# Performance work log

Hardware: AMD Instinct MI355X
Metric: run time of the kernel (lower is better)

The kernel has to match this reference:

```python
import jax, jax.numpy as jnp
import numpy as np

TAU = 0.07
EPS = 1e-6
LN_EPS = 1e-5  # torch nn.LayerNorm default
NORM_EPS = 1e-12  # torch F.normalize default


def _l2norm(x):
    n = jnp.sqrt(jnp.sum(x * x, axis=-1, keepdims=True))
    return x / jnp.maximum(n, NORM_EPS)


def setup_inputs() -> dict:
    key = jax.random.key(0)
    k1, k2, k3, k4 = jax.random.split(key, 4)
    B, N, D, K = 16, 2048, 512, 8
    f_raw = jax.random.normal(k1, (B, N, D), dtype=jnp.float32)
    f_q = jax.random.normal(k2, (B, D), dtype=jnp.float32)
    gt_mask = jax.random.randint(k3, (B, N), 0, 2) > 0
    q_bg = jax.random.normal(k4, (K, D), dtype=jnp.float32) * 0.02
    alpha = jnp.float32(1.0)
    ln_w = jnp.ones((D,), dtype=jnp.float32)
    ln_b = jnp.zeros((D,), dtype=jnp.float32)
    return {"f_raw": f_raw, "f_q": f_q, "gt_mask": gt_mask,
            "q_bg": q_bg, "alpha": alpha, "ln_w": ln_w, "ln_b": ln_b}


def reference(f_raw, f_q, gt_mask, q_bg, alpha, ln_w, ln_b):
    B, N, D = f_raw.shape
    # background prototypes via cross-attention (K queries)
    attn = jax.nn.softmax(jnp.einsum('kd,bnd->bkn', q_bg, f_raw) / jnp.sqrt(jnp.float32(D)), axis=-1)
    p_bg = jnp.einsum('bkn,bnd->bkd', attn, f_raw)  # [B,K,D]
    # projection of each token onto each prototype, summed (einsum instead of (B,N,K,D) broadcast)
    numer = jnp.einsum('bnd,bkd->bnk', f_raw, p_bg)
    denom = jnp.sum(p_bg * p_bg, axis=-1) + EPS        # [B,K]
    coef = numer / denom[:, None, :]                   # [B,N,K]
    f_bg = jnp.einsum('bnk,bkd->bnd', coef, p_bg)      # [B,N,D]
    # foreground = LayerNorm(f_raw - alpha * f_bg)
    x = f_raw - alpha * f_bg
    mu = jnp.mean(x, axis=-1, keepdims=True)
    var = jnp.mean((x - mu) ** 2, axis=-1, keepdims=True)
    f_fg = (x - mu) / jnp.sqrt(var + LN_EPS) * ln_w + ln_b
    # semantic scores vs query embedding
    sim = jnp.sum(_l2norm(f_fg) * _l2norm(f_q)[:, None, :], axis=-1)
    s_sem = jax.nn.sigmoid(sim / TAU)
    # compactness: min cosine distance of each token to a prototype
    dot = jnp.einsum('bnd,bkd->bnk', _l2norm(f_raw), _l2norm(p_bg))
    loss_compact = jnp.mean(jnp.min(1.0 - dot, axis=-1))
    # orthogonality: off-diagonal gram of normalized f_bg ([B,N,N])
    p_n = _l2norm(f_bg)
    gram = jnp.einsum('bnd,bmd->bnm', p_n, p_n)
    eye = jnp.eye(N, dtype=gram.dtype)[None]
    loss_orth = jnp.mean((gram * (1.0 - eye)) ** 2)
    # alignment: -log of positive scores (masked mean)
    m = gt_mask.astype(s_sem.dtype)
    cnt = jnp.sum(m)
    neg_log = -jnp.log(jnp.maximum(s_sem, EPS))
    loss_align = jnp.where(cnt > 0, jnp.sum(neg_log * m) / jnp.maximum(cnt, 1.0), 0.0)
    return f_fg, f_bg, p_bg, s_sem, loss_compact, loss_orth, loss_align
```

## Files before the change

kernel.cpp:

```cpp
#include <hip/hip_runtime.h>
#include <math.h>

#define Bb 16
#define Nn 2048
#define Dd 512
#define Kk 8

constexpr float TAU = 0.07f;
constexpr float EPSc = 1e-6f;
constexpr float LN_EPS = 1e-5f;
constexpr float NORM_EPS = 1e-12f;
constexpr float SCALE = 0.04419417382415922f;

constexpr size_t OUT_FFG  = 0;
constexpr size_t OUT_FBG  = (size_t)Bb*Nn*Dd;
constexpr size_t OUT_PBG  = OUT_FBG + (size_t)Bb*Nn*Dd;
constexpr size_t OUT_SSEM = OUT_PBG + (size_t)Bb*Kk*Dd;
constexpr size_t OUT_LOSS = OUT_SSEM + (size_t)Bb*Nn;

constexpr int    NCH = 64;
constexpr size_t WS_PBPART = 0;
constexpr size_t WS_SUMW   = WS_PBPART + (size_t)Bb*NCH*Kk*Dd;
constexpr size_t WS_NF2    = WS_SUMW + (size_t)Bb*NCH*Kk;
constexpr size_t WS_SF     = WS_NF2 + (size_t)Bb*Nn;
constexpr size_t WS_M      = WS_SF + (size_t)Bb*Nn;
constexpr size_t WS_IDEN   = WS_M + Bb*64;
constexpr size_t WS_INP    = WS_IDEN + Bb*Kk;
constexpr size_t WS_P1     = WS_INP + Bb*Kk;
constexpr size_t WS_FQN    = WS_P1 + Bb*Kk;
constexpr size_t WS_CP     = WS_FQN + (size_t)Bb*Dd;
constexpr size_t WS_P5A    = WS_CP + (size_t)Bb*Nn*Kk;
constexpr size_t WS_P5B    = WS_P5A + 2048;
constexpr size_t WS_TRB    = WS_P5B + 2048;

__device__ __forceinline__ float dot4(float4 a, float4 b) {
    return a.x*b.x + a.y*b.y + a.z*b.z + a.w*b.w;
}
__device__ __forceinline__ float4 add4(float4 a, float4 b) {
    return make_float4(a.x+b.x, a.y+b.y, a.z+b.z, a.w+b.w);
}
__device__ __forceinline__ float4 shfl_xor4(float4 v, int m) {
    return make_float4(__shfl_xor(v.x,m,64), __shfl_xor(v.y,m,64),
                       __shfl_xor(v.z,m,64), __shfl_xor(v.w,m,64));
}
__device__ __forceinline__ float4 shfl4(float4 v, int src) {
    return make_float4(__shfl(v.x,src,64), __shfl(v.y,src,64),
                       __shfl(v.z,src,64), __shfl(v.w,src,64));
}

__global__ __launch_bounds__(512, 4) void k1_scores(const float* __restrict__ f_raw,
                                                    const float* __restrict__ q_bg,
                                                    float* __restrict__ ws) {
    int b = blockIdx.x >> 6;
    int chunk = blockIdx.x & 63;
    int tok0 = chunk * 32;
    int tid = threadIdx.x, lane = tid & 63, wave = tid >> 6;
    __shared__ float qls[Kk*Dd];
    __shared__ float part[8][32][12];
    __shared__ float wlds[32][8];
    __shared__ float swsum[8][8];
    for (int e = tid; e < Kk*Dd; e += 512) qls[e] = q_bg[e];
    __syncthreads();
    int tok = lane & 31, half = lane >> 5;
    int dwl = wave*64 + half*32;
    const float* ftok = f_raw + ((size_t)b*Nn + tok0 + tok)*Dd + dwl;

    float a[8] = {0,0,0,0,0,0,0,0};
    float nf2 = 0.f, sf = 0.f;
    #pragma unroll
    for (int cc = 0; cc < 8; ++cc) {
        float4 f4 = *(const float4*)(ftok + cc*4);
        int qo = dwl + cc*4;
        #pragma unroll
        for (int k = 0; k < 8; ++k) {
            float4 q4 = *(const float4*)&qls[k*Dd + qo];
            a[k] += dot4(f4, q4);
        }
        nf2 += dot4(f4, f4);
        sf  += f4.x + f4.y + f4.z + f4.w;
    }
    #pragma unroll
    for (int k = 0; k < 8; ++k) a[k] += __shfl_xor(a[k], 32, 64);
    nf2 += __shfl_xor(nf2, 32, 64);
    sf  += __shfl_xor(sf, 32, 64);
    if (lane < 32) {
        *(float4*)&part[wave][tok][0] = make_float4(a[0],a[1],a[2],a[3]);
        *(float4*)&part[wave][tok][4] = make_float4(a[4],a[5],a[6],a[7]);
        *(float2*)&part[wave][tok][8] = make_float2(nf2, sf);
    }
    __syncthreads();
    {
        int sub = lane >> 4, idx = lane & 15;
        int pw = idx >> 1, hh = idx & 1;
        int tokl = wave*4 + sub;
        float4 Av = *(const float4*)&part[pw][tokl][hh*4];
        Av = add4(Av, shfl_xor4(Av, 2));
        Av = add4(Av, shfl_xor4(Av, 4));
        Av = add4(Av, shfl_xor4(Av, 8));
        int gbase = lane & 48;
        float4 Alo = shfl4(Av, gbase);
        float4 Ahi = shfl4(Av, gbase + 1);
        float n2 = (idx < 8) ? part[idx][tokl][8] : 0.f;
        float s1 = (idx < 8) ? part[idx][tokl][9] : 0.f;
        #pragma unroll
        for (int m = 1; m <= 8; m <<= 1) {
            n2 += __shfl_xor(n2, m, 64);
            s1 += __shfl_xor(s1, m, 64);
        }
        float w8[8];
        w8[0]=expf(Alo.x*SCALE); w8[1]=expf(Alo.y*SCALE);
        w8[2]=expf(Alo.z*SCALE); w8[3]=expf(Alo.w*SCALE);
        w8[4]=expf(Ahi.x*SCALE); w8[5]=expf(Ahi.y*SCALE);
        w8[6]=expf(Ahi.z*SCALE); w8[7]=expf(Ahi.w*SCALE);
        if (idx == 0) {
            size_t n = (size_t)b*Nn + tok0 + tokl;
            ws[WS_NF2 + n] = n2;
            ws[WS_SF + n]  = s1;
            *(float4*)&wlds[tokl][0] = make_float4(w8[0],w8[1],w8[2],w8[3]);
            *(float4*)&wlds[tokl][4] = make_float4(w8[4],w8[5],w8[6],w8[7]);
        }
        float4 wl = (idx == 0) ? make_float4(w8[0],w8[1],w8[2],w8[3]) : make_float4(0,0,0,0);
        float4 wh = (idx == 0) ? make_float4(w8[4],w8[5],w8[6],w8[7]) : make_float4(0,0,0,0);
        wl = add4(wl, shfl_xor4(wl, 16)); wl = add4(wl, shfl_xor4(wl, 32));
        wh = add4(wh, shfl_xor4(wh, 16)); wh = add4(wh, shfl_xor4(wh, 32));
        if (lane == 0) {
            *(float4*)&swsum[wave][0] = wl;
            *(float4*)&swsum[wave][4] = wh;
        }
    }
    __syncthreads();
    if (tid < 8) {
        float s = 0.f;
        #pragma unroll
        for (int w = 0; w < 8; ++w) s += swsum[w][tid];
        ws[WS_SUMW + (size_t)(b*NCH + chunk)*8 + tid] = s;
    }
    int d = tid;
    const float* fcol = f_raw + ((size_t)b*Nn + tok0)*Dd + d;
    float acc[8] = {0,0,0,0,0,0,0,0};
    #pragma unroll 4
    for (int nn = 0; nn < 32; ++nn) {
        float f = fcol[(size_t)nn*Dd];
        float4 wa = *(const float4*)&wlds[nn][0];
        float4 wb = *(const float4*)&wlds[nn][4];
        acc[0]+=wa.x*f; acc[1]+=wa.y*f; acc[2]+=wa.z*f; acc[3]+=wa.w*f;
        acc[4]+=wb.x*f; acc[5]+=wb.y*f; acc[6]+=wb.z*f; acc[7]+=wb.w*f;
    }
    #pragma unroll
    for (int k = 0; k < 8; ++k)
        ws[WS_PBPART + ((size_t)(b*NCH + chunk)*8 + k)*Dd + d] = acc[k];
}

__global__ __launch_bounds__(256) void k3b1_reduce(float* __restrict__ ws,
                                                   float* __restrict__ out_pbg) {
    int b = blockIdx.x, k = blockIdx.y;
    int tid = threadIdx.x;
    float v = ws[WS_SUMW + (size_t)(b*NCH + (tid & 63))*8 + k];
    #pragma unroll
    for (int off = 32; off >= 1; off >>= 1) v += __shfl_xor(v, off, 64);
    float swt = 1.f / v;
    float s0 = 0.f, s1 = 0.f;
    #pragma unroll 4
    for (int ns = 0; ns < NCH; ++ns) {
        const float* p = ws + WS_PBPART + ((size_t)(b*NCH + ns)*8 + k)*Dd;
        s0 += p[tid];
        s1 += p[tid + 256];
    }
    out_pbg[(size_t)b*Kk*Dd + (size_t)k*Dd + tid]       = s0*swt;
    out_pbg[(size_t)b*Kk*Dd + (size_t)k*Dd + tid + 256] = s1*swt;
}

__global__ __launch_bounds__(256) void k3b2_stats(float* __restrict__ ws,
                                                  const float* __restrict__ pbg,
                                                  const float* __restrict__ f_q) {
    int b = blockIdx.x, tid = threadIdx.x;
    int lane = tid & 63, wave = tid >> 6;
    __shared__ float pb[Kk*Dd];
    __shared__ float mseg[64][4];
    __shared__ float p1seg[8][8];
    __shared__ float red[4];
    for (int e = tid; e < Kk*Dd; e += 256) pb[e] = pbg[(size_t)b*Kk*Dd + e];
    float q0 = f_q[b*Dd + tid], q1 = f_q[b*Dd + 256 + tid];
    float p2 = q0*q0 + q1*q1;
    #pragma unroll
    for (int off = 32; off >= 1; off >>= 1) p2 += __shfl_xor(p2, off, 64);
    if (lane == 0) red[wave] = p2;
    __syncthreads();
    float invq = 1.f/fmaxf(sqrtf(red[0]+red[1]+red[2]+red[3]), NORM_EPS);
    ws[WS_FQN + b*Dd + tid] = q0*invq;
    ws[WS_FQN + b*Dd + 256 + tid] = q1*invq;
    {
        int pair = tid >> 2, seg = tid & 3;
        int i = pair >> 3, j = pair & 7;
        float s = 0.f;
        for (int d = seg*128; d < seg*128 + 128; ++d) s += pb[i*Dd + d]*pb[j*Dd + d];
        mseg[pair][seg] = s;
    }
    if (tid < 64) {
        int k = tid >> 3, sg = tid & 7;
        float s1 = 0.f;
        for (int d = sg*64; d < sg*64 + 64; ++d) s1 += pb[k*Dd + d];
        p1seg[k][sg] = s1;
    }
    __syncthreads();
    if (tid < 64) {
        float m = mseg[tid][0] + mseg[tid][1] + mseg[tid][2] + mseg[tid][3];
        ws[WS_M + b*64 + tid] = m;
        if ((tid >> 3) == (tid & 7)) {
            int k = tid & 7;
            ws[WS_IDEN + b*Kk + k] = 1.f/(m + EPSc);
            ws[WS_INP + b*Kk + k] = 1.f/fmaxf(sqrtf(m), NORM_EPS);
        }
    }
    if (tid < 8) {
        float s1 = 0.f;
        #pragma unroll
        for (int sg = 0; sg < 8; ++sg) s1 += p1seg[tid][sg];
        ws[WS_P1 + b*Kk + tid] = s1;
    }
}

__global__ __launch_bounds__(512, 4) void k5_main(
    const float* __restrict__ f_raw, const int* __restrict__ gt_mask,
    const float* __restrict__ alpha_p, const float* __restrict__ ln_w,
    const float* __restrict__ ln_b, const float* __restrict__ pbg,
    float* __restrict__ ws, float* __restrict__ out_ffg,
    float* __restrict__ out_fbg, float* __restrict__ out_ssem)
{
    int b = blockIdx.x >> 6;
    int chunk = blockIdx.x & 63;
    int tok0 = chunk * 32;
    int tid = threadIdx.x, lane = tid & 63, wave = tid >> 6;
    __shared__ float pls[Kk*Dd];
    __shared__ float part[8][32][8];
    __shared__ float scl[32][12];
    __shared__ float Ml[64];
    __shared__ float idenl[8], inpl[8], p1l[8];
    __shared__ float al[8][4];
    for (int e = tid; e < Kk*Dd; e += 512) pls[e] = pbg[(size_t)b*Kk*Dd + e];
    if (tid >= 512-96 && tid < 512-32) Ml[tid-(512-96)] = ws[WS_M + b*64 + (tid-(512-96))];
    else if (tid >= 512-32 && tid < 512-8) {
        int g = (tid-(512-32)) >> 3, k = (tid-(512-32)) & 7;
        if      (g == 0) idenl[k] = ws[WS_IDEN + b*8 + k];
        else if (g == 1) inpl[k]  = ws[WS_INP  + b*8 + k];
        else             p1l[k]   = ws[WS_P1   + b*8 + k];
    }
    __syncthreads();
    int tok = lane & 31, half = lane >> 5;
    int dwl = wave*64 + half*32;
    const float* ftok = f_raw + ((size_t)b*Nn + tok0 + tok)*Dd + dwl;

    float a[8] = {0,0,0,0,0,0,0,0};
    #pragma unroll
    for (int cc = 0; cc < 8; ++cc) {
        float4 f4 = *(const float4*)(ftok + cc*4);
        int po = dwl + cc*4;
        #pragma unroll
        for (int k = 0; k < 8; ++k) {
            float4 p4 = *(const float4*)&pls[k*Dd + po];
            a[k] += dot4(f4, p4);
        }
    }
    #pragma unroll
    for (int k = 0; k < 8; ++k) a[k] += __shfl_xor(a[k], 32, 64);
    if (lane < 32) {
        *(float4*)&part[wave][tok][0] = make_float4(a[0],a[1],a[2],a[3]);
        *(float4*)&part[wave][tok][4] = make_float4(a[4],a[5],a[6],a[7]);
    }
    __syncthreads();
    float wcsum, wdsum;
    {
        int sub = lane >> 4, idx = lane & 15;
        int pw = idx >> 1, hh = idx & 1;
        int tokl = wave*4 + sub;
        float4 Av = *(const float4*)&part[pw][tokl][hh*4];
        Av = add4(Av, shfl_xor4(Av, 2));
        Av = add4(Av, shfl_xor4(Av, 4));
        Av = add4(Av, shfl_xor4(Av, 8));
        int gbase = lane & 48;
        float4 Alo = shfl4(Av, gbase);
        float4 Ahi = shfl4(Av, gbase + 1);
        float A[8] = {Alo.x, Alo.y, Alo.z, Alo.w, Ahi.x, Ahi.y, Ahi.z, Ahi.w};
        size_t n = (size_t)b*Nn + tok0 + tokl;
        float nf2 = ws[WS_NF2 + n];
        float sf  = ws[WS_SF + n];
        float alpha = alpha_p[0];
        float coef[8], sca = 0.f, sp1 = 0.f;
        #pragma unroll
        for (int k = 0; k < 8; ++k) {
            coef[k] = A[k]*idenl[k];
            sca += coef[k]*A[k];
            sp1 += coef[k]*p1l[k];
        }
        float quad = 0.f;
        #pragma unroll
        for (int i = 0; i < 8; ++i) {
            float ti = 0.f;
            #pragma unroll
            for (int j = 0; j < 8; ++j) ti += Ml[i*8+j]*coef[j];
            quad += coef[i]*ti;
        }
        float sx  = sf - alpha*sp1;
        float sxx = nf2 - 2.f*alpha*sca + alpha*alpha*quad;
        float mu  = sx*(1.f/Dd);
        float var = sxx*(1.f/Dd) - mu*mu;
        float rstd = 1.f/sqrtf(fmaxf(var, 0.f) + LN_EPS);
        float invnf = 1.f/fmaxf(sqrtf(nf2), NORM_EPS);
        float cmin = 1e30f;
        #pragma unroll
        for (int k = 0; k < 8; ++k) cmin = fminf(cmin, 1.f - A[k]*invnf*inpl[k]);
        float invnb = 1.f/fmaxf(sqrtf(quad), NORM_EPS);
        float inb2 = invnb*invnb;
        float gnn = quad*inb2;
        float dloc = gnn*gnn;
        if (idx == 0) {
            *(float4*)&scl[tokl][0] = make_float4(coef[0],coef[1],coef[2],coef[3]);
            *(float4*)&scl[tokl][4] = make_float4(coef[4],coef[5],coef[6],coef[7]);
            *(float2*)&scl[tokl][8] = make_float2(mu, rstd);
            *(float4*)(ws + WS_CP + n*8)     = make_float4(coef[0]*invnb,coef[1]*invnb,coef[2]*invnb,coef[3]*invnb);
            *(float4*)(ws + WS_CP + n*8 + 4) = make_float4(coef[4]*invnb,coef[5]*invnb,coef[6]*invnb,coef[7]*invnb);
        }
        float cv = (idx == 0) ? cmin : 0.f;
        float dv = (idx == 0) ? dloc : 0.f;
        cv += __shfl_xor(cv, 16, 64); cv += __shfl_xor(cv, 32, 64);
        dv += __shfl_xor(dv, 16, 64); dv += __shfl_xor(dv, 32, 64);
        wcsum = cv; wdsum = dv;
    }
    float alpha = alpha_p[0];
    float ng2h[4], dqh[4];
    {
        int d0 = lane*4;
        float4 pbr[8];
        #pragma unroll
        for (int k = 0; k < 8; ++k) pbr[k] = *(const float4*)&pls[k*Dd + d0];
        float4 w4 = *(const float4*)(ln_w + d0);
        float4 b4 = *(const float4*)(ln_b + d0);
        float4 q4 = *(const float4*)(ws + WS_FQN + b*Dd + d0);
        #pragma unroll
        for (int t = 0; t < 4; ++t) {
            int lt = wave*4 + t;
            float4 cA = *(const float4*)&scl[lt][0];
            float4 cB = *(const float4*)&scl[lt][4];
            float2 mr = *(const float2*)&scl[lt][8];
            size_t rowoff = ((size_t)b*Nn + tok0 + lt)*Dd;
            float4 fv = *(const float4*)(f_raw + rowoff + d0);
            float4 fb;
            fb.x = cA.x*pbr[0].x + cA.y*pbr[1].x + cA.z*pbr[2].x + cA.w*pbr[3].x
                 + cB.x*pbr[4].x + cB.y*pbr[5].x + cB.z*pbr[6].x + cB.w*pbr[7].x;
            fb.y = cA.x*pbr[0].y + cA.y*pbr[1].y + cA.z*pbr[2].y + cA.w*pbr[3].y
                 + cB.x*pbr[4].y + cB.y*pbr[5].y + cB.z*pbr[6].y + cB.w*pbr[7].y;
            fb.z = cA.x*pbr[0].z + cA.y*pbr[1].z + cA.z*pbr[2].z + cA.w*pbr[3].z
                 + cB.x*pbr[4].z + cB.y*pbr[5].z + cB.z*pbr[6].z + cB.w*pbr[7].z;
            fb.w = cA.x*pbr[0].w + cA.y*pbr[1].w + cA.z*pbr[2].w + cA.w*pbr[3].w
                 + cB.x*pbr[4].w + cB.y*pbr[5].w + cB.z*pbr[6].w + cB.w*pbr[7].w;
            *(float4*)(out_fbg + rowoff + d0) = fb;
            float4 g;
            g.x = (fv.x - alpha*fb.x - mr.x)*mr.y*w4.x + b4.x;
            g.y = (fv.y - alpha*fb.y - mr.x)*mr.y*w4.y + b4.y;
            g.z = (fv.z - alpha*fb.z - mr.x)*mr.y*w4.z + b4.z;
            g.w = (fv.w - alpha*fb.w - mr.x)*mr.y*w4.w + b4.w;
            *(float4*)(out_ffg + rowoff + d0) = g;
            ng2h[t] = dot4(g, g);
            dqh[t]  = dot4(g, q4);
        }
    }
    float align_s = 0.f, align_c = 0.f;
    {
        int d0 = 256 + lane*4;
        float4 pbr[8];
        #pragma unroll
        for (int k = 0; k < 8; ++k) pbr[k] = *(const float4*)&pls[k*Dd + d0];
        float4 w4 = *(const float4*)(ln_w + d0);
        float4 b4 = *(const float4*)(ln_b + d0);
        float4 q4 = *(const float4*)(ws + WS_FQN + b*Dd + d0);
        #pragma unroll
        for (int t = 0; t < 4; ++t) {
            int lt = wave*4 + t;
            size_t n = (size_t)b*Nn + tok0 + lt;
            float4 cA = *(const float4*)&scl[lt][0];
            float4 cB = *(const float4*)&scl[lt][4];
            float2 mr = *(const float2*)&scl[lt][8];
            size_t rowoff = n*(size_t)Dd;
            float4 fv = *(const float4*)(f_raw + rowoff + d0);
            float4 fb;
            fb.x = cA.x*pbr[0].x + cA.y*pbr[1].x + cA.z*pbr[2].x + cA.w*pbr[3].x
                 + cB.x*pbr[4].x + cB.y*pbr[5].x + cB.z*pbr[6].x + cB.w*pbr[7].x;
            fb.y = cA.x*pbr[0].y + cA.y*pbr[1].y + cA.z*pbr[2].y + cA.w*pbr[3].y
                 + cB.x*pbr[4].y + cB.y*pbr[5].y + cB.z*pbr[6].y + cB.w*pbr[7].y;
            fb.z = cA.x*pbr[0].z + cA.y*pbr[1].z + cA.z*pbr[2].z + cA.w*pbr[3].z
                 + cB.x*pbr[4].z + cB.y*pbr[5].z + cB.z*pbr[6].z + cB.w*pbr[7].z;
            fb.w = cA.x*pbr[0].w + cA.y*pbr[1].w + cA.z*pbr[2].w + cA.w*pbr[3].w
                 + cB.x*pbr[4].w + cB.y*pbr[5].w + cB.z*pbr[6].w + cB.w*pbr[7].w;
            *(float4*)(out_fbg + rowoff + d0) = fb;
            float4 g;
            g.x = (fv.x - alpha*fb.x - mr.x)*mr.y*w4.x + b4.x;
            g.y = (fv.y - alpha*fb.y - mr.x)*mr.y*w4.y + b4.y;
            g.z = (fv.z - alpha*fb.z - mr.x)*mr.y*w4.z + b4.z;
            g.w = (fv.w - alpha*fb.w - mr.x)*mr.y*w4.w + b4.w;
            *(float4*)(out_ffg + rowoff + d0) = g;
            float ng2 = ng2h[t] + dot4(g, g);
            float dq  = dqh[t]  + dot4(g, q4);
            #pragma unroll
            for (int off = 32; off >= 1; off >>= 1) {
                ng2 += __shfl_xor(ng2, off, 64);
                dq  += __shfl_xor(dq,  off, 64);
            }
            float sim = dq * (1.f/fmaxf(sqrtf(ng2), NORM_EPS));
            float ssem = 1.f/(1.f + expf(-sim*(1.f/TAU)));
            if (lane == 0) {
                out_ssem[n] = ssem;
                if (gt_mask[n] != 0) { align_s += -logf(fmaxf(ssem, EPSc)); align_c += 1.f; }
            }
        }
    }
    if (lane == 0) {
        al[wave][0] = align_s; al[wave][1] = align_c;
        al[wave][2] = wcsum;   al[wave][3] = wdsum;
    }
    __syncthreads();
    if (tid == 0) {
        float as = 0.f, ac = 0.f, cs = 0.f, ds = 0.f;
        #pragma unroll
        for (int w = 0; w < 8; ++w) {
            as += al[w][0]; ac += al[w][1]; cs += al[w][2]; ds += al[w][3];
        }
        ws[WS_P5B + (size_t)blockIdx.x*2 + 0] = as;
        ws[WS_P5B + (size_t)blockIdx.x*2 + 1] = ac;
        ws[WS_P5A + (size_t)blockIdx.x*2 + 0] = cs;
        ws[WS_P5A + (size_t)blockIdx.x*2 + 1] = ds;
    }
}

__global__ __launch_bounds__(256) void k6s_gram(float* __restrict__ ws) {
    int b = blockIdx.x, tid = threadIdx.x;
    __shared__ float cps[256*8];
    __shared__ float Sred[4][64];
    __shared__ float Sfull[64];
    __shared__ float Alds[64];
    __shared__ float Mlds[64];
    int pr = tid & 63, g = tid >> 6;
    int i = pr >> 3, j = pr & 7;
    float s = 0.f;
    for (int tile = 0; tile < 8; ++tile) {
        __syncthreads();
        #pragma unroll
        for (int q = 0; q < 2; ++q)
            *(float4*)&cps[tid*8 + q*4] =
                *(const float4*)(ws + WS_CP + ((size_t)b*Nn + tile*256)*8 + tid*8 + q*4);
        __syncthreads();
        for (int nn = g*64; nn < g*64 + 64; ++nn)
            s += cps[nn*8 + i]*cps[nn*8 + j];
    }
    Sred[g][pr] = s;
    if (tid < 64) Mlds[tid] = ws[WS_M + b*64 + tid];
    __syncthreads();
    if (tid < 64) Sfull[tid] = Sred[0][tid]+Sred[1][tid]+Sred[2][tid]+Sred[3][tid];
    __syncthreads();
    if (tid < 64) {
        int ii = tid >> 3, jj = tid & 7;
        float a = 0.f;
        #pragma unroll
        for (int k = 0; k < 8; ++k) a += Mlds[ii*8+k]*Sfull[k*8+jj];
        Alds[tid] = a;
    }
    __syncthreads();
    if (tid < 64) {
        float p = Alds[tid]*Alds[(tid & 7)*8 + (tid >> 3)];
        #pragma unroll
        for (int off = 32; off >= 1; off >>= 1) p += __shfl_xor(p, off, 64);
        if (tid == 0) ws[WS_TRB + b] = p;
    }
}

__global__ __launch_bounds__(256) void k7_final(const float* __restrict__ ws,
                                                float* __restrict__ out_loss) {
    int tid = threadIdx.x, lane = tid & 63, wave = tid >> 6;
    __shared__ double red[4][4];
    double c = 0.0, dg = 0.0, as = 0.0, ac = 0.0;
    for (int idx = tid; idx < 1024; idx += 256) {
        c  += (double)ws[WS_P5A + idx*2 + 0];
        dg += (double)ws[WS_P5A + idx*2 + 1];
        as += (double)ws[WS_P5B + idx*2 + 0];
        ac += (double)ws[WS_P5B + idx*2 + 1];
    }
    #pragma unroll
    for (int off = 32; off >= 1; off >>= 1) {
        c  += __shfl_xor(c,  off, 64);
        dg += __shfl_xor(dg, off, 64);
        as += __shfl_xor(as, off, 64);
        ac += __shfl_xor(ac, off, 64);
    }
    if (lane == 0) { red[wave][0]=c; red[wave][1]=dg; red[wave][2]=as; red[wave][3]=ac; }
    __syncthreads();
    if (tid == 0) {
        double ct=0, dgt=0, ast=0, act=0, trt=0;
        for (int w = 0; w < 4; ++w) { ct+=red[w][0]; dgt+=red[w][1]; ast+=red[w][2]; act+=red[w][3]; }
        for (int b = 0; b < Bb; ++b) trt += (double)ws[WS_TRB + b];
        out_loss[0] = (float)(ct / (double)((size_t)Bb*Nn));
        out_loss[1] = (float)((trt - dgt) / ((double)Bb*(double)Nn*(double)Nn));
        out_loss[2] = (float)(act > 0.0 ? ast / (act > 1.0 ? act : 1.0) : 0.0);
    }
}

extern "C" void kernel_launch(void* const* d_in, const int* in_sizes, int n_in,
                              void* d_out, int out_size, void* d_ws, size_t ws_size,
                              hipStream_t stream) {
    (void)in_sizes; (void)n_in; (void)out_size; (void)ws_size;
    const float* f_raw   = (const float*)d_in[0];
    const float* f_q     = (const float*)d_in[1];
    const int*   gt_mask = (const int*)d_in[2];
    const float* q_bg    = (const float*)d_in[3];
    const float* alpha   = (const float*)d_in[4];
    const float* ln_w    = (const float*)d_in[5];
    const float* ln_b    = (const float*)d_in[6];
    float* out = (float*)d_out;
    float* ws  = (float*)d_ws;

    k1_scores<<<Bb*NCH, 512, 0, stream>>>(f_raw, q_bg, ws);
    k3b1_reduce<<<dim3(Bb, Kk), 256, 0, stream>>>(ws, out + OUT_PBG);
    k3b2_stats<<<Bb, 256, 0, stream>>>(ws, out + OUT_PBG, f_q);
    k5_main<<<Bb*NCH, 512, 0, stream>>>(f_raw, gt_mask, alpha, ln_w, ln_b,
                                        out + OUT_PBG, ws,
                                        out + OUT_FFG, out + OUT_FBG, out + OUT_SSEM);
    k6s_gram<<<Bb, 256, 0, stream>>>(ws);
    k7_final<<<1, 256, 0, stream>>>(ws, out + OUT_LOSS);
}
```

Before: 120.1 us.

## Remap token dot-products to 16-lane groups with shuffle reduction; use nontemporal output stores

```diff
diff --git a/kernel.cpp b/kernel.cpp
--- a/kernel.cpp
+++ b/kernel.cpp
@@ -36,16 +36,11 @@
 __device__ __forceinline__ float dot4(float4 a, float4 b) {
     return a.x*b.x + a.y*b.y + a.z*b.z + a.w*b.w;
 }
-__device__ __forceinline__ float4 add4(float4 a, float4 b) {
-    return make_float4(a.x+b.x, a.y+b.y, a.z+b.z, a.w+b.w);
-}
-__device__ __forceinline__ float4 shfl_xor4(float4 v, int m) {
-    return make_float4(__shfl_xor(v.x,m,64), __shfl_xor(v.y,m,64),
-                       __shfl_xor(v.z,m,64), __shfl_xor(v.w,m,64));
-}
-__device__ __forceinline__ float4 shfl4(float4 v, int src) {
-    return make_float4(__shfl(v.x,src,64), __shfl(v.y,src,64),
-                       __shfl(v.z,src,64), __shfl(v.w,src,64));
+
+using f32x4 = __attribute__((ext_vector_type(4))) float;
+__device__ __forceinline__ void nt_store4(float* p, float4 v) {
+    f32x4 t; t.x = v.x; t.y = v.y; t.z = v.z; t.w = v.w;
+    __builtin_nontemporal_store(t, (f32x4*)p);
 }
 
 __global__ __launch_bounds__(512, 4) void k1_scores(const float* __restrict__ f_raw,
@@ -56,77 +51,56 @@
     int tok0 = chunk * 32;
     int tid = threadIdx.x, lane = tid & 63, wave = tid >> 6;
     __shared__ float qls[Kk*Dd];
-    __shared__ float part[8][32][12];
     __shared__ float wlds[32][8];
     __shared__ float swsum[8][8];
     for (int e = tid; e < Kk*Dd; e += 512) qls[e] = q_bg[e];
     __syncthreads();
-    int tok = lane & 31, half = lane >> 5;
-    int dwl = wave*64 + half*32;
-    const float* ftok = f_raw + ((size_t)b*Nn + tok0 + tok)*Dd + dwl;
+    int sub = lane >> 4, idx = lane & 15;
+    int tokl = wave*4 + sub;
+    const float* ftok = f_raw + ((size_t)b*Nn + tok0 + tokl)*Dd;
 
     float a[8] = {0,0,0,0,0,0,0,0};
     float nf2 = 0.f, sf = 0.f;
     #pragma unroll
     for (int cc = 0; cc < 8; ++cc) {
-        float4 f4 = *(const float4*)(ftok + cc*4);
-        int qo = dwl + cc*4;
+        int o = cc*64 + idx*4;
+        float4 f4 = *(const float4*)(ftok + o);
         #pragma unroll
         for (int k = 0; k < 8; ++k) {
-            float4 q4 = *(const float4*)&qls[k*Dd + qo];
+            float4 q4 = *(const float4*)&qls[k*Dd + o];
             a[k] += dot4(f4, q4);
         }
         nf2 += dot4(f4, f4);
         sf  += f4.x + f4.y + f4.z + f4.w;
     }
     #pragma unroll
-    for (int k = 0; k < 8; ++k) a[k] += __shfl_xor(a[k], 32, 64);
-    nf2 += __shfl_xor(nf2, 32, 64);
-    sf  += __shfl_xor(sf, 32, 64);
-    if (lane < 32) {
-        *(float4*)&part[wave][tok][0] = make_float4(a[0],a[1],a[2],a[3]);
-        *(float4*)&part[wave][tok][4] = make_float4(a[4],a[5],a[6],a[7]);
-        *(float2*)&part[wave][tok][8] = make_float2(nf2, sf);
-    }
-    __syncthreads();
-    {
-        int sub = lane >> 4, idx = lane & 15;
-        int pw = idx >> 1, hh = idx & 1;
-        int tokl = wave*4 + sub;
-        float4 Av = *(const float4*)&part[pw][tokl][hh*4];
-        Av = add4(Av, shfl_xor4(Av, 2));
-        Av = add4(Av, shfl_xor4(Av, 4));
-        Av = add4(Av, shfl_xor4(Av, 8));
-        int gbase = lane & 48;
-        float4 Alo = shfl4(Av, gbase);
-        float4 Ahi = shfl4(Av, gbase + 1);
-        float n2 = (idx < 8) ? part[idx][tokl][8] : 0.f;
-        float s1 = (idx < 8) ? part[idx][tokl][9] : 0.f;
-        #pragma unroll
-        for (int m = 1; m <= 8; m <<= 1) {
-            n2 += __shfl_xor(n2, m, 64);
-            s1 += __shfl_xor(s1, m, 64);
-        }
-        float w8[8];
-        w8[0]=expf(Alo.x*SCALE); w8[1]=expf(Alo.y*SCALE);
-        w8[2]=expf(Alo.z*SCALE); w8[3]=expf(Alo.w*SCALE);
-        w8[4]=expf(Ahi.x*SCALE); w8[5]=expf(Ahi.y*SCALE);
-        w8[6]=expf(Ahi.z*SCALE); w8[7]=expf(Ahi.w*SCALE);
-        if (idx == 0) {
-            size_t n = (size_t)b*Nn + tok0 + tokl;
-            ws[WS_NF2 + n] = n2;
-            ws[WS_SF + n]  = s1;
-            *(float4*)&wlds[tokl][0] = make_float4(w8[0],w8[1],w8[2],w8[3]);
-            *(float4*)&wlds[tokl][4] = make_float4(w8[4],w8[5],w8[6],w8[7]);
-        }
-        float4 wl = (idx == 0) ? make_float4(w8[0],w8[1],w8[2],w8[3]) : make_float4(0,0,0,0);
-        float4 wh = (idx == 0) ? make_float4(w8[4],w8[5],w8[6],w8[7]) : make_float4(0,0,0,0);
-        wl = add4(wl, shfl_xor4(wl, 16)); wl = add4(wl, shfl_xor4(wl, 32));
-        wh = add4(wh, shfl_xor4(wh, 16)); wh = add4(wh, shfl_xor4(wh, 32));
-        if (lane == 0) {
-            *(float4*)&swsum[wave][0] = wl;
-            *(float4*)&swsum[wave][4] = wh;
-        }
+    for (int m = 1; m <= 8; m <<= 1) {
+        #pragma unroll
+        for (int k = 0; k < 8; ++k) a[k] += __shfl_xor(a[k], m, 64);
+        nf2 += __shfl_xor(nf2, m, 64);
+        sf  += __shfl_xor(sf, m, 64);
+    }
+    float w8[8];
+    #pragma unroll
+    for (int k = 0; k < 8; ++k) w8[k] = expf(a[k]*SCALE);
+    if (idx == 0) {
+        size_t n = (size_t)b*Nn + tok0 + tokl;
+        ws[WS_NF2 + n] = nf2;
+        ws[WS_SF + n]  = sf;
+        *(float4*)&wlds[tokl][0] = make_float4(w8[0],w8[1],w8[2],w8[3]);
+        *(float4*)&wlds[tokl][4] = make_float4(w8[4],w8[5],w8[6],w8[7]);
+    }
+    float sw[8];
+    #pragma unroll
+    for (int k = 0; k < 8; ++k) sw[k] = (idx == 0) ? w8[k] : 0.f;
+    #pragma unroll
+    for (int k = 0; k < 8; ++k) {
+        sw[k] += __shfl_xor(sw[k], 16, 64);
+        sw[k] += __shfl_xor(sw[k], 32, 64);
+    }
+    if (lane == 0) {
+        *(float4*)&swsum[wave][0] = make_float4(sw[0],sw[1],sw[2],sw[3]);
+        *(float4*)&swsum[wave][4] = make_float4(sw[4],sw[5],sw[6],sw[7]);
     }
     __syncthreads();
     if (tid < 8) {
@@ -232,7 +206,6 @@
     int tok0 = chunk * 32;
     int tid = threadIdx.x, lane = tid & 63, wave = tid >> 6;
     __shared__ float pls[Kk*Dd];
-    __shared__ float part[8][32][8];
     __shared__ float scl[32][12];
     __shared__ float Ml[64];
     __shared__ float idenl[8], inpl[8], p1l[8];
@@ -246,41 +219,28 @@
         else             p1l[k]   = ws[WS_P1   + b*8 + k];
     }
     __syncthreads();
-    int tok = lane & 31, half = lane >> 5;
-    int dwl = wave*64 + half*32;
-    const float* ftok = f_raw + ((size_t)b*Nn + tok0 + tok)*Dd + dwl;
-
-    float a[8] = {0,0,0,0,0,0,0,0};
+    int sub = lane >> 4, idx = lane & 15;
+    int tokl = wave*4 + sub;
+    const float* ftok = f_raw + ((size_t)b*Nn + tok0 + tokl)*Dd;
+
+    float A[8] = {0,0,0,0,0,0,0,0};
     #pragma unroll
     for (int cc = 0; cc < 8; ++cc) {
-        float4 f4 = *(const float4*)(ftok + cc*4);
-        int po = dwl + cc*4;
+        int o = cc*64 + idx*4;
+        float4 f4 = *(const float4*)(ftok + o);
         #pragma unroll
         for (int k = 0; k < 8; ++k) {
-            float4 p4 = *(const float4*)&pls[k*Dd + po];
-            a[k] += dot4(f4, p4);
-        }
-    }
-    #pragma unroll
-    for (int k = 0; k < 8; ++k) a[k] += __shfl_xor(a[k], 32, 64);
-    if (lane < 32) {
-        *(float4*)&part[wave][tok][0] = make_float4(a[0],a[1],a[2],a[3]);
-        *(float4*)&part[wave][tok][4] = make_float4(a[4],a[5],a[6],a[7]);
-    }
-    __syncthreads();
+            float4 p4 = *(const float4*)&pls[k*Dd + o];
+            A[k] += dot4(f4, p4);
+        }
+    }
+    #pragma unroll
+    for (int m = 1; m <= 8; m <<= 1) {
+        #pragma unroll
+        for (int k = 0; k < 8; ++k) A[k] += __shfl_xor(A[k], m, 64);
+    }
     float wcsum, wdsum;
     {
-        int sub = lane >> 4, idx = lane & 15;
-        int pw = idx >> 1, hh = idx & 1;
-        int tokl = wave*4 + sub;
-        float4 Av = *(const float4*)&part[pw][tokl][hh*4];
-        Av = add4(Av, shfl_xor4(Av, 2));
-        Av = add4(Av, shfl_xor4(Av, 4));
-        Av = add4(Av, shfl_xor4(Av, 8));
-        int gbase = lane & 48;
-        float4 Alo = shfl4(Av, gbase);
-        float4 Ahi = shfl4(Av, gbase + 1);
-        float A[8] = {Alo.x, Alo.y, Alo.z, Alo.w, Ahi.x, Ahi.y, Ahi.z, Ahi.w};
         size_t n = (size_t)b*Nn + tok0 + tokl;
         float nf2 = ws[WS_NF2 + n];
         float sf  = ws[WS_SF + n];
@@ -353,13 +313,13 @@
                  + cB.x*pbr[4].z + cB.y*pbr[5].z + cB.z*pbr[6].z + cB.w*pbr[7].z;
             fb.w = cA.x*pbr[0].w + cA.y*pbr[1].w + cA.z*pbr[2].w + cA.w*pbr[3].w
                  + cB.x*pbr[4].w + cB.y*pbr[5].w + cB.z*pbr[6].w + cB.w*pbr[7].w;
-            *(float4*)(out_fbg + rowoff + d0) = fb;
+            nt_store4(out_fbg + rowoff + d0, fb);
             float4 g;
             g.x = (fv.x - alpha*fb.x - mr.x)*mr.y*w4.x + b4.x;
             g.y = (fv.y - alpha*fb.y - mr.x)*mr.y*w4.y + b4.y;
             g.z = (fv.z - alpha*fb.z - mr.x)*mr.y*w4.z + b4.z;
             g.w = (fv.w - alpha*fb.w - mr.x)*mr.y*w4.w + b4.w;
-            *(float4*)(out_ffg + rowoff + d0) = g;
+            nt_store4(out_ffg + rowoff + d0, g);
             ng2h[t] = dot4(g, g);
             dqh[t]  = dot4(g, q4);
         }
@@ -391,13 +351,13 @@
                  + cB.x*pbr[4].z + cB.y*pbr[5].z + cB.z*pbr[6].z + cB.w*pbr[7].z;
             fb.w = cA.x*pbr[0].w + cA.y*pbr[1].w + cA.z*pbr[2].w + cA.w*pbr[3].w
                  + cB.x*pbr[4].w + cB.y*pbr[5].w + cB.z*pbr[6].w + cB.w*pbr[7].w;
-            *(float4*)(out_fbg + rowoff + d0) = fb;
+            nt_store4(out_fbg + rowoff + d0, fb);
             float4 g;
             g.x = (fv.x - alpha*fb.x - mr.x)*mr.y*w4.x + b4.x;
             g.y = (fv.y - alpha*fb.y - mr.x)*mr.y*w4.y + b4.y;
             g.z = (fv.z - alpha*fb.z - mr.x)*mr.y*w4.z + b4.z;
             g.w = (fv.w - alpha*fb.w - mr.x)*mr.y*w4.w + b4.w;
-            *(float4*)(out_ffg + rowoff + d0) = g;
+            nt_store4(out_ffg + rowoff + d0, g);
             float ng2 = ng2h[t] + dot4(g, g);
             float dq  = dqh[t]  + dot4(g, q4);
             #pragma unroll
```

After: 109.4 us. 1.1x faster.
